# Kernel tuning notes

Measured on AMD Instinct MI355X. Metric: run time of the kernel, lower is better.

Reference implementation:

```python
import jax, jax.numpy as jnp
import numpy as np

B, S, F, DK = 4, 2048, 1024, 1024

def setup_inputs() -> dict:
    key = jax.random.key(0)
    ks = jax.random.split(key, 9)
    sF = 1.0 / np.sqrt(F)
    sD = 1.0 / np.sqrt(DK)
    return {
        "x":  jax.random.normal(ks[0], (B, S, F), dtype=jnp.float32),
        "Wq": jax.random.normal(ks[1], (DK, F), dtype=jnp.float32) * sF,
        "bq": jax.random.normal(ks[2], (DK,), dtype=jnp.float32) * sF,
        "Wk": jax.random.normal(ks[3], (DK, F), dtype=jnp.float32) * sF,
        "bk": jax.random.normal(ks[4], (DK,), dtype=jnp.float32) * sF,
        "Wv": jax.random.normal(ks[5], (DK, F), dtype=jnp.float32) * sF,
        "bv": jax.random.normal(ks[6], (DK,), dtype=jnp.float32) * sF,
        "Wo": jax.random.normal(ks[7], (F, DK), dtype=jnp.float32) * sD,
        "bo": jax.random.normal(ks[8], (F,), dtype=jnp.float32) * sD,
    }

def reference(x, Wq, bq, Wk, bk, Wv, bv, Wo, bo):
    # Linear layers (torch convention: y = x @ W.T + b)
    q = jnp.einsum('bsf,df->bsd', x, Wq) + bq  # (B,S,DK)
    k = jnp.einsum('bsf,df->bsd', x, Wk) + bk  # (B,S,DK)
    v = jnp.einsum('bsf,df->bsd', x, Wv) + bv  # (B,S,DK)
    scale = 1.0 / (q.shape[-1] ** 0.5)
    scores = jnp.einsum('bqd,bkd->bqk', q, k) * scale  # (B,Sq,Sk)
    # Faithful to original: softmax over dim=-2 (the QUERY axis)
    attn = jax.nn.softmax(scores, axis=-2)
    ctx = jnp.einsum('bqk,bkd->bqd', attn, v)  # (B,S,DK)
    out = jnp.einsum('bsd,fd->bsf', ctx, Wo) + bo  # (B,S,F)
    return out
```

## Files before the change

### kernel.cpp

```cpp
#include <hip/hip_runtime.h>
#include <hip/hip_bf16.h>
#include <math.h>

typedef __bf16 bf16_t;
typedef __bf16 bf16x8 __attribute__((ext_vector_type(8)));
typedef float f32x4 __attribute__((ext_vector_type(4)));


__device__ __forceinline__ void g2l16(const bf16_t* g, bf16_t* l) {
  __builtin_amdgcn_global_load_lds(
      (const __attribute__((address_space(1))) void*)g,
      (__attribute__((address_space(3))) void*)l, 16, 0, 0);
}

__device__ __forceinline__ float waveSum(float v) {
#pragma unroll
  for (int o = 32; o > 0; o >>= 1) v += __shfl_xor(v, o);
  return v;
}

__device__ __forceinline__ void xcdswz(int& bx, int& by, int& bz) {
  const int gx = gridDim.x, gy = gridDim.y;
  const int n = gx * gy * gridDim.z;
  int f = bx + gx * (by + gy * bz);
  const int cpx = n >> 3;
  int s = (f & 7) * cpx + (f >> 3);
  bx = s % gx; s /= gx; by = s % gy; bz = s / gy;
}

__device__ __forceinline__ bf16x8 rdf(const char* base, int row, int kbyte) {
  int off = (row << 7) + kbyte;
  off ^= (row & 7) << 4;
  return *reinterpret_cast<const bf16x8*>(base + off);
}


__global__ __launch_bounds__(256) void cast_f32_to_bf16(
    const float* __restrict__ in, bf16_t* __restrict__ out, long n) {
  long i = ((long)blockIdx.x * 256 + threadIdx.x) * 8;
  if (i >= n) return;
  float4 a = *reinterpret_cast<const float4*>(in + i);
  float4 b = *reinterpret_cast<const float4*>(in + i + 4);
  bf16x8 o;
  o[0] = (bf16_t)a.x; o[1] = (bf16_t)a.y; o[2] = (bf16_t)a.z; o[3] = (bf16_t)a.w;
  o[4] = (bf16_t)b.x; o[5] = (bf16_t)b.y; o[6] = (bf16_t)b.z; o[7] = (bf16_t)b.w;
  *reinterpret_cast<bf16x8*>(out + i) = o;
}

__global__ __launch_bounds__(256) void cast_w4(
    const float* __restrict__ w0, const float* __restrict__ w1,
    const float* __restrict__ w2, const float* __restrict__ w3,
    bf16_t* __restrict__ o0, bf16_t* __restrict__ o1,
    bf16_t* __restrict__ o2, bf16_t* __restrict__ o3) {
  const int sel = blockIdx.x >> 9;
  const int blk = blockIdx.x & 511;
  const float* in = sel == 0 ? w0 : (sel == 1 ? w1 : (sel == 2 ? w2 : w3));
  bf16_t* out = sel == 0 ? o0 : (sel == 1 ? o1 : (sel == 2 ? o2 : o3));
  long i = ((long)blk * 256 + threadIdx.x) * 8;
  float4 a = *reinterpret_cast<const float4*>(in + i);
  float4 b = *reinterpret_cast<const float4*>(in + i + 4);
  bf16x8 o;
  o[0] = (bf16_t)a.x; o[1] = (bf16_t)a.y; o[2] = (bf16_t)a.z; o[3] = (bf16_t)a.w;
  o[4] = (bf16_t)b.x; o[5] = (bf16_t)b.y; o[6] = (bf16_t)b.z; o[7] = (bf16_t)b.w;
  *reinterpret_cast<bf16x8*>(out + i) = o;
}


#define STAGE256(d, o, h, t) do {                                              \
  const bf16_t* gsrc_ = ((o) ? Bb : Ab) + (long)((h) * 128 + srl) * K +        \
                        (long)(t) * 64 + sgsw;                                 \
  bf16_t* ldsb_ = &lds[d][o][(h) * 8192] + ldst;                               \
  g2l16(gsrc_, ldsb_);                                                         \
  g2l16(gsrc_ + 64L * K, ldsb_ + 4096);                                        \
} while (0)

#define AREAD256(d, qm) do {                                                   \
  const char* Ab_ = (const char*)&lds[d][0][0];                                \
  int r_ = (qm) * 128 + wr2 * 64 + rA;                                         \
  a0 = rdf(Ab_, r_, kb);      a1 = rdf(Ab_, r_, kb + 64);                      \
  a2 = rdf(Ab_, r_ + 16, kb); a3 = rdf(Ab_, r_ + 16, kb + 64);                 \
  a4 = rdf(Ab_, r_ + 32, kb); a5 = rdf(Ab_, r_ + 32, kb + 64);                 \
  a6 = rdf(Ab_, r_ + 48, kb); a7 = rdf(Ab_, r_ + 48, kb + 64);                 \
} while (0)

#define BREAD256(d, qn, r0v, r1v, r2v, r3v) do {                               \
  const char* Bb_ = (const char*)&lds[d][1][0];                                \
  int c_ = (qn) * 128 + wc2 * 32 + rA;                                         \
  r0v = rdf(Bb_, c_, kb);      r1v = rdf(Bb_, c_, kb + 64);                    \
  r2v = rdf(Bb_, c_ + 16, kb); r3v = rdf(Bb_, c_ + 16, kb + 64);               \
} while (0)

#define MFMA16(qm, qn, b0v, b1v, b2v, b3v) do {                                \
  acc[(qm)*4+0][(qn)*2+0] = __builtin_amdgcn_mfma_f32_16x16x32_bf16(a0, b0v, acc[(qm)*4+0][(qn)*2+0], 0,0,0); \
  acc[(qm)*4+0][(qn)*2+0] = __builtin_amdgcn_mfma_f32_16x16x32_bf16(a1, b1v, acc[(qm)*4+0][(qn)*2+0], 0,0,0); \
  acc[(qm)*4+1][(qn)*2+0] = __builtin_amdgcn_mfma_f32_16x16x32_bf16(a2, b0v, acc[(qm)*4+1][(qn)*2+0], 0,0,0); \
  acc[(qm)*4+1][(qn)*2+0] = __builtin_amdgcn_mfma_f32_16x16x32_bf16(a3, b1v, acc[(qm)*4+1][(qn)*2+0], 0,0,0); \
  acc[(qm)*4+2][(qn)*2+0] = __builtin_amdgcn_mfma_f32_16x16x32_bf16(a4, b0v, acc[(qm)*4+2][(qn)*2+0], 0,0,0); \
  acc[(qm)*4+2][(qn)*2+0] = __builtin_amdgcn_mfma_f32_16x16x32_bf16(a5, b1v, acc[(qm)*4+2][(qn)*2+0], 0,0,0); \
  acc[(qm)*4+3][(qn)*2+0] = __builtin_amdgcn_mfma_f32_16x16x32_bf16(a6, b0v, acc[(qm)*4+3][(qn)*2+0], 0,0,0); \
  acc[(qm)*4+3][(qn)*2+0] = __builtin_amdgcn_mfma_f32_16x16x32_bf16(a7, b1v, acc[(qm)*4+3][(qn)*2+0], 0,0,0); \
  acc[(qm)*4+0][(qn)*2+1] = __builtin_amdgcn_mfma_f32_16x16x32_bf16(a0, b2v, acc[(qm)*4+0][(qn)*2+1], 0,0,0); \
  acc[(qm)*4+0][(qn)*2+1] = __builtin_amdgcn_mfma_f32_16x16x32_bf16(a1, b3v, acc[(qm)*4+0][(qn)*2+1], 0,0,0); \
  acc[(qm)*4+1][(qn)*2+1] = __builtin_amdgcn_mfma_f32_16x16x32_bf16(a2, b2v, acc[(qm)*4+1][(qn)*2+1], 0,0,0); \
  acc[(qm)*4+1][(qn)*2+1] = __builtin_amdgcn_mfma_f32_16x16x32_bf16(a3, b3v, acc[(qm)*4+1][(qn)*2+1], 0,0,0); \
  acc[(qm)*4+2][(qn)*2+1] = __builtin_amdgcn_mfma_f32_16x16x32_bf16(a4, b2v, acc[(qm)*4+2][(qn)*2+1], 0,0,0); \
  acc[(qm)*4+2][(qn)*2+1] = __builtin_amdgcn_mfma_f32_16x16x32_bf16(a5, b3v, acc[(qm)*4+2][(qn)*2+1], 0,0,0); \
  acc[(qm)*4+3][(qn)*2+1] = __builtin_amdgcn_mfma_f32_16x16x32_bf16(a6, b2v, acc[(qm)*4+3][(qn)*2+1], 0,0,0); \
  acc[(qm)*4+3][(qn)*2+1] = __builtin_amdgcn_mfma_f32_16x16x32_bf16(a7, b3v, acc[(qm)*4+3][(qn)*2+1], 0,0,0); \
} while (0)

#define PH_ENTER() do {                                                        \
  __builtin_amdgcn_s_barrier();                                                \
  asm volatile("s_waitcnt lgkmcnt(0)" ::: "memory");                           \
  __builtin_amdgcn_sched_barrier(0);                                           \
  __builtin_amdgcn_s_setprio(1);                                               \
} while (0)

#define PH_EXIT() do {                                                         \
  __builtin_amdgcn_s_setprio(0);                                               \
  __builtin_amdgcn_s_barrier();                                                \
  __builtin_amdgcn_sched_barrier(0);                                           \
} while (0)

template <int EPI>
__launch_bounds__(512, 2)
__global__ void gemm256(const bf16_t* __restrict__ A, const bf16_t* __restrict__ B,
                        int K, float alpha,
                        void* __restrict__ C0, void* __restrict__ C1, void* __restrict__ C2,
                        const float* __restrict__ bias0, const float* __restrict__ bias1,
                        const float* __restrict__ bias2,
                        int Ncols, long sA, long sB, long sC) {
  __shared__ bf16_t lds[2][2][16384];

  int bx = blockIdx.x, by = blockIdx.y, bz = blockIdx.z;
  xcdswz(bx, by, bz);

  const int tid = threadIdx.x;
  const int lane = tid & 63;
  const int w = tid >> 6;
  const int wr2 = w >> 2;
  const int wc2 = w & 3;
  const int rA = lane & 15;
  const int kb = (lane >> 4) << 4;

  const int bm = bx * 256;
  const int bn = by * 256;
  const bf16_t* Ab = A + (long)bz * sA + (long)bm * K;
  const bf16_t* Bb = B + (long)bz * sB + (long)bn * K;

  const int srl = tid >> 3;
  const int sgr = tid & 7;
  const int sgsw = (sgr ^ (srl & 7)) * 8;
  const int ldst = srl * 64 + sgr * 8;

  f32x4 acc[8][4] = {};
  bf16x8 a0, a1, a2, a3, a4, a5, a6, a7;
  bf16x8 p0, p1, p2, p3, q0, q1, q2, q3;

  const int NT = K >> 6;

  STAGE256(0, 0, 0, 0); STAGE256(0, 1, 0, 0);
  STAGE256(0, 0, 1, 0); STAGE256(0, 1, 1, 0);
  STAGE256(1, 0, 0, 1); STAGE256(1, 1, 0, 1);
  asm volatile("s_waitcnt vmcnt(4)" ::: "memory");
  __builtin_amdgcn_s_barrier();
  __builtin_amdgcn_sched_barrier(0);

  int t = 0;
  for (int it = 0; it < NT / 2 - 1; ++it, t += 2) {
    AREAD256(0, 0); BREAD256(0, 0, p0, p1, p2, p3);
    STAGE256(1, 0, 1, t + 1);
    PH_ENTER(); MFMA16(0, 0, p0, p1, p2, p3); PH_EXIT();
    BREAD256(0, 1, q0, q1, q2, q3);
    STAGE256(1, 1, 1, t + 1);
    PH_ENTER(); MFMA16(0, 1, q0, q1, q2, q3); PH_EXIT();
    AREAD256(0, 1);
    STAGE256(0, 0, 0, t + 2);
    PH_ENTER(); MFMA16(1, 0, p0, p1, p2, p3); PH_EXIT();
    STAGE256(0, 1, 0, t + 2);
    asm volatile("s_waitcnt vmcnt(4)" ::: "memory");
    PH_ENTER(); MFMA16(1, 1, q0, q1, q2, q3); PH_EXIT();
    AREAD256(1, 0); BREAD256(1, 0, p0, p1, p2, p3);
    STAGE256(0, 0, 1, t + 2);
    PH_ENTER(); MFMA16(0, 0, p0, p1, p2, p3); PH_EXIT();
    BREAD256(1, 1, q0, q1, q2, q3);
    STAGE256(0, 1, 1, t + 2);
    PH_ENTER(); MFMA16(0, 1, q0, q1, q2, q3); PH_EXIT();
    AREAD256(1, 1);
    STAGE256(1, 0, 0, t + 3);
    PH_ENTER(); MFMA16(1, 0, p0, p1, p2, p3); PH_EXIT();
    STAGE256(1, 1, 0, t + 3);
    asm volatile("s_waitcnt vmcnt(4)" ::: "memory");
    PH_ENTER(); MFMA16(1, 1, q0, q1, q2, q3); PH_EXIT();
  }

  AREAD256(0, 0); BREAD256(0, 0, p0, p1, p2, p3);
  STAGE256(1, 0, 1, t + 1);
  PH_ENTER(); MFMA16(0, 0, p0, p1, p2, p3); PH_EXIT();
  BREAD256(0, 1, q0, q1, q2, q3);
  STAGE256(1, 1, 1, t + 1);
  PH_ENTER(); MFMA16(0, 1, q0, q1, q2, q3); PH_EXIT();
  AREAD256(0, 1);
  PH_ENTER(); MFMA16(1, 0, p0, p1, p2, p3); PH_EXIT();
  asm volatile("s_waitcnt vmcnt(0)" ::: "memory");
  PH_ENTER(); MFMA16(1, 1, q0, q1, q2, q3); PH_EXIT();
  AREAD256(1, 0); BREAD256(1, 0, p0, p1, p2, p3);
  PH_ENTER(); MFMA16(0, 0, p0, p1, p2, p3); PH_EXIT();
  BREAD256(1, 1, q0, q1, q2, q3);
  PH_ENTER(); MFMA16(0, 1, q0, q1, q2, q3); PH_EXIT();
  AREAD256(1, 1);
  PH_ENTER(); MFMA16(1, 0, p0, p1, p2, p3); PH_EXIT();
  PH_ENTER(); MFMA16(1, 1, q0, q1, q2, q3); PH_EXIT();

  const int rr = (lane >> 4) * 4;
  const int cc = lane & 15;
#pragma unroll
  for (int qm = 0; qm < 2; ++qm)
#pragma unroll
    for (int m = 0; m < 4; ++m) {
      const int grow = bm + qm * 128 + wr2 * 64 + m * 16 + rr;
#pragma unroll
      for (int qn = 0; qn < 2; ++qn)
#pragma unroll
        for (int n = 0; n < 2; ++n) {
          const int gcol = bn + qn * 128 + wc2 * 32 + n * 16 + cc;
          const f32x4 v = acc[qm * 4 + m][qn * 2 + n];
          if (EPI == 1) {
            const int sel = gcol >> 10;
            const int lcol = gcol & 1023;
            const float* bp = sel == 0 ? bias0 : (sel == 1 ? bias1 : bias2);
            bf16_t* op = sel == 0 ? (bf16_t*)C0 : (sel == 1 ? (bf16_t*)C1 : (bf16_t*)C2);
            const float bv = bp[lcol];
#pragma unroll
            for (int j = 0; j < 4; ++j)
              op[(long)(grow + j) * 1024 + lcol] = (bf16_t)(v[j] + bv);
          } else {
            bf16_t* C = (bf16_t*)C0 + (long)bz * sC;
#pragma unroll
            for (int j = 0; j < 4; ++j)
              C[(long)(grow + j) * Ncols + gcol] = (bf16_t)__expf(v[j] * alpha);
          }
        }
    }
  (void)Ncols;
}


template <int OUT_BF16, int HAS_BIAS>
__launch_bounds__(256, 2)
__global__ void gemm_bt(const bf16_t* __restrict__ A, const bf16_t* __restrict__ B,
                        const float* __restrict__ bias, void* __restrict__ Cv,
                        int M, int N, int K, float alpha,
                        long sA, long sB, long sC) {
  int bxi = blockIdx.x, byi = blockIdx.y, bzi = blockIdx.z;
  xcdswz(bxi, byi, bzi);
  const bf16_t* Ab = A + (long)bzi * sA;
  const bf16_t* Bb = B + (long)bzi * sB;
  const int bm = bxi * 128;
  const int bn = byi * 128;

  __shared__ bf16_t sAt[128 * 32];
  __shared__ bf16_t sBt[128 * 32];

  const int tid = threadIdx.x;
  const int lane = tid & 63;
  const int w = tid >> 6;
  const int wr = (w >> 1) * 64;
  const int wc = (w & 1) * 64;

  f32x4 acc[4][4] = {};

  const int r0 = tid >> 2;
  const int c0 = (tid & 3) * 8;
  const int r1 = 64 + (tid >> 2);
  const long lds0 = (long)tid * 8;
  const long lds1 = 2048 + (long)tid * 8;

  const int arow = wr + (lane & 15);
  const int brow = wc + (lane & 15);
  const int koff = (lane >> 4) * 8;

  const int nK = K >> 5;
  for (int kt = 0; kt < nK; ++kt) {
    const int k0 = kt << 5;
    g2l16(Ab + (long)(bm + r0) * K + k0 + c0, sAt + lds0);
    g2l16(Ab + (long)(bm + r1) * K + k0 + c0, sAt + lds1);
    g2l16(Bb + (long)(bn + r0) * K + k0 + c0, sBt + lds0);
    g2l16(Bb + (long)(bn + r1) * K + k0 + c0, sBt + lds1);
    __syncthreads();

    bf16x8 af[4], bfr[4];
#pragma unroll
    for (int m = 0; m < 4; ++m)
      af[m] = *reinterpret_cast<const bf16x8*>(sAt + (arow + m * 16) * 32 + koff);
#pragma unroll
    for (int n = 0; n < 4; ++n)
      bfr[n] = *reinterpret_cast<const bf16x8*>(sBt + (brow + n * 16) * 32 + koff);
#pragma unroll
    for (int m = 0; m < 4; ++m)
#pragma unroll
      for (int n = 0; n < 4; ++n)
        acc[m][n] = __builtin_amdgcn_mfma_f32_16x16x32_bf16(af[m], bfr[n], acc[m][n], 0, 0, 0);
    __syncthreads();
  }

  const int rbase = bm + wr + (lane >> 4) * 4;
  const int cbase = bn + wc + (lane & 15);
#pragma unroll
  for (int n = 0; n < 4; ++n) {
    const int col = cbase + n * 16;
    float bv = 0.f;
    if (HAS_BIAS) bv = bias[col];
#pragma unroll
    for (int m = 0; m < 4; ++m) {
      const int row0 = rbase + m * 16;
#pragma unroll
      for (int j = 0; j < 4; ++j) {
        float v = acc[m][n][j] * alpha + bv;
        if (OUT_BF16) {
          bf16_t* C = (bf16_t*)Cv + (long)bzi * sC;
          C[(long)(row0 + j) * N + col] = (bf16_t)v;
        } else {
          float* C = (float*)Cv + (long)bzi * sC;
          C[(long)(row0 + j) * N + col] = v;
        }
      }
    }
  }
}


__global__ __launch_bounds__(256) void row_sums(const bf16_t* __restrict__ P,
                                                float* __restrict__ rinv) {
  const long row = blockIdx.x;
  const bf16_t* p = P + row * 2048;
  const int t = threadIdx.x;
  bf16x8 a = *reinterpret_cast<const bf16x8*>(p + t * 8);
  float s = 0.f;
#pragma unroll
  for (int u = 0; u < 8; ++u) s += (float)a[u];
  s = waveSum(s);
  __shared__ float red[4];
  if ((t & 63) == 0) red[t >> 6] = s;
  __syncthreads();
  s = red[0] + red[1] + red[2] + red[3];
  if (t == 0) rinv[row] = 1.0f / s;
}


__global__ __launch_bounds__(256) void scale_T(const bf16_t* __restrict__ P,
                                               const float* __restrict__ rinv,
                                               bf16_t* __restrict__ attn) {
  const int b = blockIdx.z;
  const int q0 = blockIdx.x * 64;
  const int kk0 = blockIdx.y * 64;
  __shared__ bf16_t tile[64][72];
  const int t = threadIdx.x;
  const int i = t >> 2;
  const int qj = (t & 3) * 16;
  const long grow = (long)b * 2048 + kk0 + i;
  const float ri = rinv[grow];
  const bf16_t* src = P + grow * 2048 + q0 + qj;
  bf16x8 v0 = *reinterpret_cast<const bf16x8*>(src);
  bf16x8 v1 = *reinterpret_cast<const bf16x8*>(src + 8);
#pragma unroll
  for (int u = 0; u < 8; ++u) {
    tile[i][qj + u] = (bf16_t)((float)v0[u] * ri);
    tile[i][qj + 8 + u] = (bf16_t)((float)v1[u] * ri);
  }
  __syncthreads();
  const int j = t >> 2;
  const int kc = (t & 3) * 16;
  bf16x8 o0, o1;
#pragma unroll
  for (int u = 0; u < 8; ++u) o0[u] = tile[kc + u][j];
#pragma unroll
  for (int u = 0; u < 8; ++u) o1[u] = tile[kc + 8 + u][j];
  bf16_t* dst = attn + ((long)b * 2048 + q0 + j) * 2048 + kk0 + kc;
  *reinterpret_cast<bf16x8*>(dst) = o0;
  *reinterpret_cast<bf16x8*>(dst + 8) = o1;
}


__global__ __launch_bounds__(256) void transpose_bf16k(const bf16_t* __restrict__ in,
                                                       bf16_t* __restrict__ out,
                                                       int R, int C) {
  const int b = blockIdx.z;
  const int r0 = blockIdx.x * 64;
  const int c0 = blockIdx.y * 64;
  __shared__ bf16_t tile[64][72];
  const int t = threadIdx.x;
  const int i = t >> 2;
  const int cj = (t & 3) * 16;
  const bf16_t* src = in + ((long)b * R + r0 + i) * C + c0 + cj;
  bf16x8 a0 = *reinterpret_cast<const bf16x8*>(src);
  bf16x8 a1 = *reinterpret_cast<const bf16x8*>(src + 8);
#pragma unroll
  for (int u = 0; u < 8; ++u) { tile[i][cj + u] = a0[u]; tile[i][cj + 8 + u] = a1[u]; }
  __syncthreads();
  const int j = t >> 2;
  const int rc = (t & 3) * 16;
  bf16x8 o0, o1;
#pragma unroll
  for (int u = 0; u < 8; ++u) o0[u] = tile[rc + u][j];
#pragma unroll
  for (int u = 0; u < 8; ++u) o1[u] = tile[rc + 8 + u][j];
  bf16_t* dst = out + ((long)b * C + c0 + j) * R + r0 + rc;
  *reinterpret_cast<bf16x8*>(dst) = o0;
  *reinterpret_cast<bf16x8*>(dst + 8) = o1;
}


extern "C" void kernel_launch(void* const* d_in, const int* in_sizes, int n_in,
                              void* d_out, int out_size, void* d_ws, size_t ws_size,
                              hipStream_t stream) {
  const float* x  = (const float*)d_in[0];
  const float* Wq = (const float*)d_in[1];
  const float* bq = (const float*)d_in[2];
  const float* Wk = (const float*)d_in[3];
  const float* bk = (const float*)d_in[4];
  const float* Wv = (const float*)d_in[5];
  const float* bv = (const float*)d_in[6];
  const float* Wo = (const float*)d_in[7];
  const float* bo = (const float*)d_in[8];
  float* out = (float*)d_out;
  char* ws = (char*)d_ws;

  const long MB = 1024L * 1024L;
  bf16_t* xb    = (bf16_t*)(ws + 0);
  bf16_t* Wqkvb = (bf16_t*)(ws + 16 * MB);
  bf16_t* Wob   = (bf16_t*)(ws + 22 * MB);
  bf16_t* Qb    = (bf16_t*)(ws + 24 * MB);
  bf16_t* Kb    = (bf16_t*)(ws + 40 * MB);
  bf16_t* Vb    = (bf16_t*)(ws + 56 * MB);
  bf16_t* Pp    = (bf16_t*)(ws + 72 * MB);
  bf16_t* attn  = (bf16_t*)(ws + 136 * MB);
  float*  rinv  = (float*)(ws + 168 * MB);
  bf16_t* VT    = (bf16_t*)(ws + 0);
  bf16_t* ctxb  = (bf16_t*)(ws + 24 * MB);

  cast_f32_to_bf16<<<4096, 256, 0, stream>>>(x, xb, 8388608);
  cast_w4<<<2048, 256, 0, stream>>>(Wq, Wk, Wv, Wo,
                                    Wqkvb, Wqkvb + 1048576, Wqkvb + 2097152, Wob);

  gemm256<1><<<dim3(32, 12, 1), 512, 0, stream>>>(
      xb, Wqkvb, 1024, 1.0f, Qb, Kb, Vb, bq, bk, bv, 3072, 0, 0, 0);

  gemm256<2><<<dim3(8, 8, 4), 512, 0, stream>>>(
      Kb, Qb, 1024, 0.03125f, Pp, nullptr, nullptr, nullptr, nullptr, nullptr,
      2048, 2048L * 1024, 2048L * 1024, 2048L * 2048);

  row_sums<<<8192, 256, 0, stream>>>(Pp, rinv);
  dim3 gsm(32, 32, 4);
  scale_T<<<gsm, 256, 0, stream>>>(Pp, rinv, attn);

  dim3 gtr(32, 16, 4);
  transpose_bf16k<<<gtr, 256, 0, stream>>>(Vb, VT, 2048, 1024);

  dim3 gctx(16, 8, 4);
  gemm_bt<1, 0><<<gctx, 256, 0, stream>>>(attn, VT, nullptr, ctxb, 2048, 1024, 2048, 1.0f,
                                          2048L * 2048, 1024L * 2048, 2048L * 1024);

  dim3 gout(64, 8, 1);
  gemm_bt<0, 1><<<gout, 256, 0, stream>>>(ctxb, Wob, bo, out, 8192, 1024, 1024, 1.0f, 0, 0, 0);

  (void)in_sizes; (void)n_in; (void)out_size; (void)ws_size;
}
```

Measured before the change: 312.8 us.

## Deepen GEMM prefetch pipeline with finer-grained vmcnt waits

Restructures the global-to-LDS staging schedule in the 256x256 GEMM so that both halves of the next k-tile are issued in the prologue, and each later tile is fetched earlier and in a different quarter order. Coarse vmcnt(4) waits are replaced with finer per-phase waits (10/12, then 8/4/2/0 in the tail). The aim is more loads in flight and less time stalled on memory before each MFMA phase. The risk is that the vmcnt counts must exactly match the STAGE issue order, otherwise LDS data races or extra stalls appear.

```diff
diff --git a/kernel.cpp b/kernel.cpp
--- a/kernel.cpp
+++ b/kernel.cpp
@@ -109,6 +109,8 @@
   acc[(qm)*4+3][(qn)*2+1] = __builtin_amdgcn_mfma_f32_16x16x32_bf16(a7, b3v, acc[(qm)*4+3][(qn)*2+1], 0,0,0); \
 } while (0)
 
+#define VMC(n) asm volatile("s_waitcnt vmcnt(" #n ")" ::: "memory")
+
 #define PH_ENTER() do {                                                        \
   __builtin_amdgcn_s_barrier();                                                \
   asm volatile("s_waitcnt lgkmcnt(0)" ::: "memory");                           \
@@ -159,54 +161,63 @@
 
   const int NT = K >> 6;
 
-  STAGE256(0, 0, 0, 0); STAGE256(0, 1, 0, 0);
-  STAGE256(0, 0, 1, 0); STAGE256(0, 1, 1, 0);
-  STAGE256(1, 0, 0, 1); STAGE256(1, 1, 0, 1);
-  asm volatile("s_waitcnt vmcnt(4)" ::: "memory");
+  STAGE256(0, 0, 0, 0);
+  STAGE256(0, 1, 0, 0);
+  STAGE256(0, 1, 1, 0);
+  STAGE256(0, 0, 1, 0);
+  STAGE256(1, 0, 0, 1);
+  STAGE256(1, 1, 0, 1);
+  STAGE256(1, 1, 1, 1);
+  STAGE256(1, 0, 1, 1);
+  VMC(12);
   __builtin_amdgcn_s_barrier();
   __builtin_amdgcn_sched_barrier(0);
 
   int t = 0;
   for (int it = 0; it < NT / 2 - 1; ++it, t += 2) {
     AREAD256(0, 0); BREAD256(0, 0, p0, p1, p2, p3);
-    STAGE256(1, 0, 1, t + 1);
+    VMC(10);
     PH_ENTER(); MFMA16(0, 0, p0, p1, p2, p3); PH_EXIT();
     BREAD256(0, 1, q0, q1, q2, q3);
-    STAGE256(1, 1, 1, t + 1);
+    STAGE256(0, 0, 0, t + 2); STAGE256(0, 1, 0, t + 2);
+    VMC(12);
     PH_ENTER(); MFMA16(0, 1, q0, q1, q2, q3); PH_EXIT();
     AREAD256(0, 1);
-    STAGE256(0, 0, 0, t + 2);
+    STAGE256(0, 1, 1, t + 2);
     PH_ENTER(); MFMA16(1, 0, p0, p1, p2, p3); PH_EXIT();
-    STAGE256(0, 1, 0, t + 2);
-    asm volatile("s_waitcnt vmcnt(4)" ::: "memory");
+    STAGE256(0, 0, 1, t + 2);
+    VMC(12);
     PH_ENTER(); MFMA16(1, 1, q0, q1, q2, q3); PH_EXIT();
     AREAD256(1, 0); BREAD256(1, 0, p0, p1, p2, p3);
-    STAGE256(0, 0, 1, t + 2);
+    VMC(10);
     PH_ENTER(); MFMA16(0, 0, p0, p1, p2, p3); PH_EXIT();
     BREAD256(1, 1, q0, q1, q2, q3);
-    STAGE256(0, 1, 1, t + 2);
+    STAGE256(1, 0, 0, t + 3); STAGE256(1, 1, 0, t + 3);
+    VMC(12);
     PH_ENTER(); MFMA16(0, 1, q0, q1, q2, q3); PH_EXIT();
     AREAD256(1, 1);
-    STAGE256(1, 0, 0, t + 3);
+    STAGE256(1, 1, 1, t + 3);
     PH_ENTER(); MFMA16(1, 0, p0, p1, p2, p3); PH_EXIT();
-    STAGE256(1, 1, 0, t + 3);
-    asm volatile("s_waitcnt vmcnt(4)" ::: "memory");
+    STAGE256(1, 0, 1, t + 3);
+    VMC(12);
     PH_ENTER(); MFMA16(1, 1, q0, q1, q2, q3); PH_EXIT();
   }
 
   AREAD256(0, 0); BREAD256(0, 0, p0, p1, p2, p3);
-  STAGE256(1, 0, 1, t + 1);
+  VMC(10);
   PH_ENTER(); MFMA16(0, 0, p0, p1, p2, p3); PH_EXIT();
   BREAD256(0, 1, q0, q1, q2, q3);
-  STAGE256(1, 1, 1, t + 1);
+  VMC(8);
   PH_ENTER(); MFMA16(0, 1, q0, q1, q2, q3); PH_EXIT();
   AREAD256(0, 1);
   PH_ENTER(); MFMA16(1, 0, p0, p1, p2, p3); PH_EXIT();
-  asm volatile("s_waitcnt vmcnt(0)" ::: "memory");
+  VMC(4);
   PH_ENTER(); MFMA16(1, 1, q0, q1, q2, q3); PH_EXIT();
   AREAD256(1, 0); BREAD256(1, 0, p0, p1, p2, p3);
+  VMC(2);
   PH_ENTER(); MFMA16(0, 0, p0, p1, p2, p3); PH_EXIT();
   BREAD256(1, 1, q0, q1, q2, q3);
+  VMC(0);
   PH_ENTER(); MFMA16(0, 1, q0, q1, q2, q3); PH_EXIT();
   AREAD256(1, 1);
   PH_ENTER(); MFMA16(1, 0, p0, p1, p2, p3); PH_EXIT();
```

Measured after the change: 313.0 us. No clear change (+0.1%).
